# Performance work log

Hardware: AMD Instinct MI355X
Metric: run time of the kernel (lower is better)

Reference implementation:

```python
import jax, jax.numpy as jnp
import numpy as np

N, D = 32768, 256  # n_nodes, in_dim == mem_dim


def setup_inputs() -> dict:
    key = jax.random.key(0)
    ks = jax.random.split(key, 8)
    inputs = jax.random.normal(ks[0], (N, D), jnp.float32)
    state = jax.random.normal(ks[1], (1, D), jnp.float32)  # initial root cell state
    s = 1.0 / np.sqrt(D)  # pytorch default uniform init bound
    root_W = jax.random.uniform(ks[2], (D, D), jnp.float32, -s, s)
    root_b = jax.random.uniform(ks[3], (D,), jnp.float32, -s, s)
    W_ih = jax.random.uniform(ks[4], (4 * D, D), jnp.float32, -s, s)
    W_hh = jax.random.uniform(ks[5], (4 * D, D), jnp.float32, -s, s)
    b_ih = jax.random.uniform(ks[6], (4 * D,), jnp.float32, -s, s)
    b_hh = jax.random.uniform(ks[7], (4 * D,), jnp.float32, -s, s)
    # topologically ordered random tree: parents[i] < i, node 0 is root
    rng = np.random.default_rng(0)
    raw = rng.integers(0, N, size=N)
    parents = jnp.asarray(np.minimum(raw, np.maximum(np.arange(N) - 1, 0)).astype(np.int64))
    idx = jnp.arange(N, dtype=jnp.int64)  # node -> input row (tree.idx)
    return dict(inputs=inputs, state=state, root_W=root_W, root_b=root_b,
                W_ih=W_ih, W_hh=W_hh, b_ih=b_ih, b_hh=b_hh,
                parents=parents, idx=idx)


def reference(inputs, state, root_W, root_b, W_ih, W_hh, b_ih, b_hh, parents, idx):
    n, d = inputs.shape
    # root: tanh(Linear(inputs[root_idx])), cell state = given state
    h0 = jnp.tanh(inputs[idx[0]] @ root_W.T + root_b)
    c0 = state[0]
    H = jnp.zeros((n, d), inputs.dtype).at[0].set(h0)
    C = jnp.zeros((n, d), inputs.dtype).at[0].set(c0)

    def step(carry, i):
        H, C = carry
        p = parents[i]
        x = inputs[idx[i]]
        # torch nn.LSTMCell: gates = x W_ih^T + b_ih + h W_hh^T + b_hh
        gates = x @ W_ih.T + b_ih + H[p] @ W_hh.T + b_hh
        ig, fg, gg, og = jnp.split(gates, 4)
        c = jax.nn.sigmoid(fg) * C[p] + jax.nn.sigmoid(ig) * jnp.tanh(gg)
        h = jax.nn.sigmoid(og) * jnp.tanh(c)
        return (H.at[i].set(h), C.at[i].set(c)), None

    (H, C), _ = jax.lax.scan(step, (H, C), jnp.arange(1, n))
    # topdown_hidden_traversal: scatter each node's hidden into a [n_inputs, mem_dim] buffer
    hiddens = jnp.zeros((n, d), inputs.dtype).at[idx].set(H)
    # (root topdown_state, root topdown hidden, all hiddens)
    return C[0:1], H[0:1], hiddens
```

## Files before the change

kernel.cpp:

```cpp
#include <hip/hip_runtime.h>


#define NN 32768
#define DD 256
#define GP 1024
#define DSTR 16

typedef __attribute__((ext_vector_type(8))) short short8;
typedef __attribute__((ext_vector_type(4))) float float4_;

static __device__ __forceinline__ unsigned short f2bf(float f) {
    unsigned u = __builtin_bit_cast(unsigned, f);
    unsigned r = u + 0x7FFFu + ((u >> 16) & 1u);
    return (unsigned short)(r >> 16);
}
static __device__ __forceinline__ float bf2f(unsigned short u) {
    unsigned v = ((unsigned)u) << 16;
    return __builtin_bit_cast(float, v);
}
static __device__ __forceinline__ float sigf(float x) { return 1.0f / (1.0f + __expf(-x)); }
static __device__ __forceinline__ float tanh_(float x) { return 1.0f - 2.0f / (__expf(2.0f * x) + 1.0f); }

__global__ void k_init(int* cnt, int* cur, int* done, int* maxd) {
    int g = blockIdx.x * 256 + threadIdx.x;
    if (g < NN + 2) { cnt[g] = 0; cur[g] = 0; }
    if (g < (NN + 2) * DSTR) done[g] = 0;
    if (g == 0) maxd[0] = 0;
}

__global__ void k_root(const float* __restrict__ X, const float* __restrict__ state,
                       const float* __restrict__ rootW, const float* __restrict__ rootb,
                       const int* __restrict__ idx,
                       unsigned short* __restrict__ Hb, float* __restrict__ C, int* __restrict__ done) {
    const int t = threadIdx.x;
    const int row = idx[0];
    const float4_* xr = (const float4_*)(X + (size_t)row * DD);
    const float4_* wr = (const float4_*)(rootW + (size_t)t * DD);
    float acc = rootb[t];
    for (int k = 0; k < DD / 4; ++k) {
        float4_ a = xr[k], b = wr[k];
        acc += a[0] * b[0] + a[1] * b[1] + a[2] * b[2] + a[3] * b[3];
    }
    Hb[t] = f2bf(tanh_(acc));
    C[t] = state[t];
    __syncthreads();
    __threadfence();
    if (t == 0) __hip_atomic_store(&done[0], 8, __ATOMIC_RELEASE, __HIP_MEMORY_SCOPE_AGENT);
}

__global__ void k_dep_init(const int* __restrict__ parents, int* dep, int* jmp) {
    int i = blockIdx.x * 256 + threadIdx.x;
    if (i >= NN) return;
    dep[i] = (i == 0) ? 0 : 1;
    jmp[i] = (i == 0) ? 0 : parents[i];
}

__global__ void k_dep_step(const int* __restrict__ depA, const int* __restrict__ jmpA,
                           int* __restrict__ depB, int* __restrict__ jmpB) {
    int i = blockIdx.x * 256 + threadIdx.x;
    if (i >= NN) return;
    int j = jmpA[i];
    depB[i] = depA[i] + depA[j];
    jmpB[i] = jmpA[j];
}

__global__ void k_hist(const int* __restrict__ dep, int* cnt, int* maxd) {
    int i = blockIdx.x * 256 + threadIdx.x;
    if (i >= NN) return;
    int d = dep[i];
    atomicAdd(&cnt[d], 1);
    atomicMax(&maxd[0], d);
}

__global__ void k_scan(const int* __restrict__ cnt, int* __restrict__ off) {
    __shared__ int sums[256];
    const int tid = threadIdx.x;
    const int base = tid * 128;
    int s = 0;
    for (int k = 0; k < 128; ++k) s += cnt[base + k];
    sums[tid] = s;
    __syncthreads();
    if (tid == 0) {
        int run = 0;
        for (int t = 0; t < 256; ++t) { int tmp = sums[t]; sums[t] = run; run += tmp; }
    }
    __syncthreads();
    int run = sums[tid];
    for (int k = 0; k < 128; ++k) { off[base + k] = run; run += cnt[base + k]; }
    if (tid == 255) off[NN] = run;
}

__global__ void k_scatter(const int* __restrict__ dep, const int* __restrict__ off,
                          int* cur, int* __restrict__ lev) {
    int i = blockIdx.x * 256 + threadIdx.x;
    if (i >= NN) return;
    int d = dep[i];
    int pos = off[d] + atomicAdd(&cur[d], 1);
    lev[pos] = i;
}

__global__ __launch_bounds__(256, 1) void k_gx(
    const float* __restrict__ X, const float* __restrict__ Wih,
    const float* __restrict__ bih, const float* __restrict__ bhh,
    const int* __restrict__ idx, unsigned short* __restrict__ Gp) {
    __shared__ __align__(16) short bw_s[128 * 264];
    __shared__ float bias_s[128];
    const int tid = threadIdx.x;
    const int w = tid >> 6, l = tid & 63;
    const int lanelo = l & 15, quad = l >> 4;

    short8 a[2][8];
    #pragma unroll
    for (int ti = 0; ti < 2; ++ti) {
        int n = (blockIdx.x * 8 + w * 2 + ti) * 16 + lanelo;
        int row = idx[n];
        const float* xp = X + (size_t)row * DD + quad * 8;
        #pragma unroll
        for (int ks = 0; ks < 8; ++ks) {
            float4_ x0 = *(const float4_*)(xp + ks * 32);
            float4_ x1 = *(const float4_*)(xp + ks * 32 + 4);
            short8 s;
            s[0] = f2bf(x0[0]); s[1] = f2bf(x0[1]); s[2] = f2bf(x0[2]); s[3] = f2bf(x0[3]);
            s[4] = f2bf(x1[0]); s[5] = f2bf(x1[1]); s[6] = f2bf(x1[2]); s[7] = f2bf(x1[3]);
            a[ti][ks] = s;
        }
    }
    for (int gc = 0; gc < 8; ++gc) {
        __syncthreads();
        for (int e = tid; e < 128 * 64; e += 256) {
            int r = e >> 6, c4 = (e & 63) * 4;
            float4_ b = *(const float4_*)(Wih + (size_t)(gc * 128 + r) * DD + c4);
            unsigned short* pb = (unsigned short*)&bw_s[r * 264 + c4];
            pb[0] = f2bf(b[0]); pb[1] = f2bf(b[1]); pb[2] = f2bf(b[2]); pb[3] = f2bf(b[3]);
        }
        if (tid < 128) bias_s[tid] = bih[gc * 128 + tid] + bhh[gc * 128 + tid];
        __syncthreads();
        #pragma unroll
        for (int ntl = 0; ntl < 8; ++ntl) {
            float4_ acc0 = (float4_){0.f, 0.f, 0.f, 0.f};
            float4_ acc1 = (float4_){0.f, 0.f, 0.f, 0.f};
            #pragma unroll
            for (int ks = 0; ks < 8; ++ks) {
                short8 bf = *(const short8*)&bw_s[(ntl * 16 + lanelo) * 264 + ks * 32 + quad * 8];
                acc0 = __builtin_amdgcn_mfma_f32_16x16x32_bf16(a[0][ks], bf, acc0, 0, 0, 0);
                acc1 = __builtin_amdgcn_mfma_f32_16x16x32_bf16(a[1][ks], bf, acc1, 0, 0, 0);
            }
            float bia = bias_s[ntl * 16 + lanelo];
            int g = gc * 128 + ntl * 16 + lanelo;
            int nb0 = (blockIdx.x * 8 + w * 2) * 16 + quad * 4;
            #pragma unroll
            for (int r = 0; r < 4; ++r) {
                Gp[(size_t)(nb0 + r) * GP + g] = f2bf(acc0[r] + bia);
                Gp[(size_t)(nb0 + 16 + r) * GP + g] = f2bf(acc1[r] + bia);
            }
        }
    }
}

__global__ __launch_bounds__(256, 1) void k_tree2(
    const float* __restrict__ Whh,
    const int* __restrict__ parents,
    const int* __restrict__ off, const int* __restrict__ lev, const int* __restrict__ maxd_g,
    const unsigned short* __restrict__ Gp,
    unsigned short* __restrict__ Hb, float* __restrict__ C, int* __restrict__ done) {

    __shared__ __align__(16) short w_s[128 * 264];
    __shared__ __align__(16) short A_s[16 * 264];
    __shared__ __align__(16) float G_s[16 * 128];
    __shared__ __align__(16) float R_s[16 * 132];
    __shared__ int nd_s[16], par_s[16];

    const int tid = threadIdx.x;
    const int j = blockIdx.x & 7, grp = blockIdx.x >> 3;
    const int w = tid >> 6, l = tid & 63;
    const int lanelo = l & 15, quad = l >> 4;

    for (int e = tid; e < 128 * 64; e += 256) {
        int r = e >> 6, c4 = (e & 63) * 4;
        int G = ((r >> 5) * 256) + j * 32 + (r & 31);
        float4_ b = *(const float4_*)(Whh + (size_t)G * DD + c4);
        unsigned short* pb = (unsigned short*)&w_s[r * 264 + c4];
        pb[0] = f2bf(b[0]); pb[1] = f2bf(b[1]); pb[2] = f2bf(b[2]); pb[3] = f2bf(b[3]);
    }
    __syncthreads();

    const int maxd = maxd_g[0];
    int prev_lo = off[0], lo = off[1];
    for (int d = 1; d <= maxd; ++d) {
        const int hi = off[d + 1];
        const int tiles = (hi - lo + 15) >> 4;
        if (grp < tiles) {
            const int target = ((lo - prev_lo + 15) >> 4) << 3;
            int ndone = 0;
            for (int t = grp; t < tiles; t += 32) {
                const int base = lo + t * 16;
                if (tid < 16) {
                    int node = -1, p = 0;
                    if (base + tid < hi) { node = lev[base + tid]; p = parents[node]; }
                    nd_s[tid] = node; par_s[tid] = p;
                }
                __syncthreads();
                {
                    int m = tid >> 4, q8 = (tid & 15) * 8;
                    int seg = q8 >> 5, cc = q8 & 31;
                    float4_ g01 = (float4_){0.f, 0.f, 0.f, 0.f};
                    float4_ g23 = (float4_){0.f, 0.f, 0.f, 0.f};
                    if (nd_s[m] >= 0) {
                        const unsigned short* gp =
                            Gp + (size_t)nd_s[m] * GP + seg * 256 + j * 32 + cc;
                        short8 gv = *(const short8*)gp;
                        g01[0] = bf2f(gv[0]); g01[1] = bf2f(gv[1]); g01[2] = bf2f(gv[2]); g01[3] = bf2f(gv[3]);
                        g23[0] = bf2f(gv[4]); g23[1] = bf2f(gv[5]); g23[2] = bf2f(gv[6]); g23[3] = bf2f(gv[7]);
                    }
                    *(float4_*)&G_s[m * 128 + q8] = g01;
                    *(float4_*)&G_s[m * 128 + q8 + 4] = g23;
                }
                if (t == grp) {
                    if (tid == 0) {
                        while (__hip_atomic_load(&done[(d - 1) * DSTR], __ATOMIC_RELAXED,
                                                 __HIP_MEMORY_SCOPE_AGENT) < target)
                            __builtin_amdgcn_s_sleep(1);
                    }
                    __syncthreads();
                    __builtin_amdgcn_fence(__ATOMIC_ACQUIRE, "workgroup");
                }
                float cp0, cp1;
                {
                    int m0 = tid >> 5, c0 = tid & 31, col = j * 32 + c0;
                    cp0 = __hip_atomic_load(&C[(size_t)par_s[m0] * DD + col],
                                            __ATOMIC_RELAXED, __HIP_MEMORY_SCOPE_AGENT);
                    cp1 = __hip_atomic_load(&C[(size_t)par_s[m0 + 8] * DD + col],
                                            __ATOMIC_RELAXED, __HIP_MEMORY_SCOPE_AGENT);
                }
                {
                    const unsigned* HbU = (const unsigned*)Hb;
                    unsigned hv[8];
                    #pragma unroll
                    for (int k2 = 0; k2 < 8; ++k2) {
                        int e = tid + k2 * 256, m = e >> 7, cu = e & 127;
                        hv[k2] = (nd_s[m] >= 0)
                            ? __hip_atomic_load(&HbU[(size_t)par_s[m] * 128 + cu],
                                                __ATOMIC_RELAXED, __HIP_MEMORY_SCOPE_AGENT)
                            : 0u;
                    }
                    #pragma unroll
                    for (int k2 = 0; k2 < 8; ++k2) {
                        int e = tid + k2 * 256, m = e >> 7, cu = e & 127;
                        *(unsigned*)&A_s[m * 264 + cu * 2] = hv[k2];
                    }
                }
                __syncthreads();
                {
                    short8 af[8];
                    #pragma unroll
                    for (int ks = 0; ks < 8; ++ks)
                        af[ks] = *(const short8*)&A_s[lanelo * 264 + ks * 32 + quad * 8];
                    #pragma unroll
                    for (int ti = 0; ti < 2; ++ti) {
                        int ntl = w * 2 + ti;
                        float4_ acc = (float4_){0.f, 0.f, 0.f, 0.f};
                        #pragma unroll
                        for (int ks = 0; ks < 8; ++ks) {
                            short8 bf = *(const short8*)&w_s[(ntl * 16 + lanelo) * 264 + ks * 32 + quad * 8];
                            acc = __builtin_amdgcn_mfma_f32_16x16x32_bf16(af[ks], bf, acc, 0, 0, 0);
                        }
                        #pragma unroll
                        for (int r = 0; r < 4; ++r)
                            R_s[(quad * 4 + r) * 132 + ntl * 16 + lanelo] = acc[r];
                    }
                }
                __syncthreads();
                {
                    int m0 = tid >> 5, c = tid & 31, col = j * 32 + c;
                    #pragma unroll
                    for (int pass = 0; pass < 2; ++pass) {
                        int m = m0 + pass * 8;
                        float cp = pass ? cp1 : cp0;
                        float ig = R_s[m * 132 + c]      + G_s[m * 128 + c];
                        float fg = R_s[m * 132 + 32 + c] + G_s[m * 128 + 32 + c];
                        float gg = R_s[m * 132 + 64 + c] + G_s[m * 128 + 64 + c];
                        float og = R_s[m * 132 + 96 + c] + G_s[m * 128 + 96 + c];
                        float cn = sigf(fg) * cp + sigf(ig) * tanh_(gg);
                        float hn = sigf(og) * tanh_(cn);
                        int node = nd_s[m];
                        unsigned short hs = f2bf(hn);
                        unsigned pair = ((unsigned)hs) |
                                        (((unsigned)(unsigned short)__shfl_down((int)hs, 1)) << 16);
                        if (node >= 0) {
                            __hip_atomic_store(&C[(size_t)node * DD + col], cn,
                                               __ATOMIC_RELAXED, __HIP_MEMORY_SCOPE_AGENT);
                            if ((c & 1) == 0)
                                __hip_atomic_store(&((unsigned*)Hb)[(size_t)node * 128 + (col >> 1)],
                                                   pair, __ATOMIC_RELAXED, __HIP_MEMORY_SCOPE_AGENT);
                        }
                    }
                }
                ndone++;
                __syncthreads();
            }
            __builtin_amdgcn_fence(__ATOMIC_RELEASE, "workgroup");
            if (tid == 0)
                __hip_atomic_fetch_add(&done[d * DSTR], ndone,
                                       __ATOMIC_RELAXED, __HIP_MEMORY_SCOPE_AGENT);
        }
        prev_lo = lo; lo = hi;
    }
}

__global__ void k_out(const unsigned short* __restrict__ Hb, const float* __restrict__ C,
                      const int* __restrict__ idx, float* __restrict__ out) {
    const int b = blockIdx.x, t = threadIdx.x;
    if (b < NN) {
        int drow = idx[b];
        out[512 + (size_t)drow * DD + t] = bf2f(Hb[(size_t)b * DD + t]);
    } else {
        out[t] = C[t];
        out[DD + t] = bf2f(Hb[t]);
    }
}

extern "C" void kernel_launch(void* const* d_in, const int* in_sizes, int n_in,
                              void* d_out, int out_size, void* d_ws, size_t ws_size,
                              hipStream_t stream) {
    const float* X     = (const float*)d_in[0];
    const float* state = (const float*)d_in[1];
    const float* rootW = (const float*)d_in[2];
    const float* rootb = (const float*)d_in[3];
    const float* Wih   = (const float*)d_in[4];
    const float* Whh   = (const float*)d_in[5];
    const float* bih   = (const float*)d_in[6];
    const float* bhh   = (const float*)d_in[7];
    const int* parents = (const int*)d_in[8];
    const int* idx     = (const int*)d_in[9];

    float* C           = (float*)d_ws;
    unsigned short* Hb = (unsigned short*)(C + (size_t)NN * DD);
    unsigned short* Gp = Hb + (size_t)NN * DD;
    int* ip            = (int*)(Gp + (size_t)NN * GP);
    int* depA = ip;            ip += NN;
    int* jmpA = ip;            ip += NN;
    int* depB = ip;            ip += NN;
    int* jmpB = ip;            ip += NN;
    int* cnt  = ip;            ip += NN + 2;
    int* off  = ip;            ip += NN + 2;
    int* cur  = ip;            ip += NN + 2;
    int* lev  = ip;            ip += NN;
    int* done = ip;            ip += (NN + 2) * DSTR;
    int* maxd = ip;            ip += 4;
    float* out = (float*)d_out;

    k_init<<<dim3(((NN + 2) * DSTR + 255) / 256), dim3(256), 0, stream>>>(cnt, cur, done, maxd);
    k_root<<<dim3(1), dim3(256), 0, stream>>>(X, state, rootW, rootb, idx, Hb, C, done);

    k_dep_init<<<dim3(128), dim3(256), 0, stream>>>(parents, depA, jmpA);
    int* dA = depA; int* jA = jmpA; int* dB = depB; int* jB = jmpB;
    for (int it = 0; it < 15; ++it) {
        k_dep_step<<<dim3(128), dim3(256), 0, stream>>>(dA, jA, dB, jB);
        int* tp;
        tp = dA; dA = dB; dB = tp;
        tp = jA; jA = jB; jB = tp;
    }
    k_hist<<<dim3(128), dim3(256), 0, stream>>>(dA, cnt, maxd);
    k_scan<<<dim3(1), dim3(256), 0, stream>>>(cnt, off);
    k_scatter<<<dim3(128), dim3(256), 0, stream>>>(dA, off, cur, lev);

    k_gx<<<dim3(256), dim3(256), 0, stream>>>(X, Wih, bih, bhh, idx, Gp);
    k_tree2<<<dim3(256), dim3(256), 0, stream>>>(Whh, parents, off, lev, maxd, Gp, Hb, C, done);
    k_out<<<dim3(NN + 1), dim3(256), 0, stream>>>(Hb, C, idx, out);
}
```

Baseline: 1.765 ms.

## Replace per-level barrier with per-tile dataflow dependency waits in tree LSTM

The tree kernel no longer waits for a whole depth level to finish before starting the next. Each 16-node tile now waits only for the specific tiles holding its nodes' parents, tracked through per-tile done counters built by new scan/scatter/tile kernels. Parent hidden states are also loaded straight into MFMA A-fragments in registers instead of being staged through shared memory, which drops a barrier. The cost is extra preprocessing kernels and per-lane polling on several counters, and there is an unused bias load added to the tree kernel.

```diff
diff --git a/kernel.cpp b/kernel.cpp
--- a/kernel.cpp
+++ b/kernel.cpp
@@ -21,17 +21,16 @@
 static __device__ __forceinline__ float sigf(float x) { return 1.0f / (1.0f + __expf(-x)); }
 static __device__ __forceinline__ float tanh_(float x) { return 1.0f - 2.0f / (__expf(2.0f * x) + 1.0f); }
 
-__global__ void k_init(int* cnt, int* cur, int* done, int* maxd) {
+__global__ void k_init(int* cnt, int* cur, int* done2) {
     int g = blockIdx.x * 256 + threadIdx.x;
     if (g < NN + 2) { cnt[g] = 0; cur[g] = 0; }
-    if (g < (NN + 2) * DSTR) done[g] = 0;
-    if (g == 0) maxd[0] = 0;
+    if (g < (NN + 2) * DSTR) done2[g] = 0;
 }
 
 __global__ void k_root(const float* __restrict__ X, const float* __restrict__ state,
                        const float* __restrict__ rootW, const float* __restrict__ rootb,
                        const int* __restrict__ idx,
-                       unsigned short* __restrict__ Hb, float* __restrict__ C, int* __restrict__ done) {
+                       unsigned short* __restrict__ Hb, float* __restrict__ C, int* __restrict__ done2) {
     const int t = threadIdx.x;
     const int row = idx[0];
     const float4_* xr = (const float4_*)(X + (size_t)row * DD);
@@ -45,7 +44,7 @@
     C[t] = state[t];
     __syncthreads();
     __threadfence();
-    if (t == 0) __hip_atomic_store(&done[0], 8, __ATOMIC_RELEASE, __HIP_MEMORY_SCOPE_AGENT);
+    if (t == 0) __hip_atomic_store(&done2[0], 8, __ATOMIC_RELEASE, __HIP_MEMORY_SCOPE_AGENT);
 }
 
 __global__ void k_dep_init(const int* __restrict__ parents, int* dep, int* jmp) {
@@ -64,39 +63,57 @@
     jmpB[i] = jmpA[j];
 }
 
-__global__ void k_hist(const int* __restrict__ dep, int* cnt, int* maxd) {
+__global__ void k_hist(const int* __restrict__ dep, int* cnt) {
     int i = blockIdx.x * 256 + threadIdx.x;
     if (i >= NN) return;
-    int d = dep[i];
-    atomicAdd(&cnt[d], 1);
-    atomicMax(&maxd[0], d);
-}
-
-__global__ void k_scan(const int* __restrict__ cnt, int* __restrict__ off) {
-    __shared__ int sums[256];
+    atomicAdd(&cnt[dep[i]], 1);
+}
+
+__global__ void k_scan2(const int* __restrict__ cnt, int* __restrict__ off,
+                        int* __restrict__ tb, int* __restrict__ nt) {
+    __shared__ int sums[256], tsums[256];
     const int tid = threadIdx.x;
     const int base = tid * 128;
-    int s = 0;
-    for (int k = 0; k < 128; ++k) s += cnt[base + k];
-    sums[tid] = s;
+    int s = 0, st = 0;
+    for (int k = 0; k < 128; ++k) { int c = cnt[base + k]; s += c; st += (c + 15) >> 4; }
+    sums[tid] = s; tsums[tid] = st;
     __syncthreads();
     if (tid == 0) {
-        int run = 0;
-        for (int t = 0; t < 256; ++t) { int tmp = sums[t]; sums[t] = run; run += tmp; }
+        int run = 0, trun = 0;
+        for (int t = 0; t < 256; ++t) {
+            int a = sums[t]; sums[t] = run; run += a;
+            int b = tsums[t]; tsums[t] = trun; trun += b;
+        }
     }
     __syncthreads();
-    int run = sums[tid];
-    for (int k = 0; k < 128; ++k) { off[base + k] = run; run += cnt[base + k]; }
-    if (tid == 255) off[NN] = run;
-}
-
-__global__ void k_scatter(const int* __restrict__ dep, const int* __restrict__ off,
-                          int* cur, int* __restrict__ lev) {
+    int run = sums[tid], trun = tsums[tid];
+    for (int k = 0; k < 128; ++k) {
+        off[base + k] = run; tb[base + k] = trun;
+        run += cnt[base + k]; trun += (cnt[base + k] + 15) >> 4;
+    }
+    if (tid == 255) { off[NN] = run; tb[NN] = trun; nt[0] = trun; }
+}
+
+__global__ void k_scatter2(const int* __restrict__ dep, const int* __restrict__ off,
+                           const int* __restrict__ tb, int* cur,
+                           int* __restrict__ lev, int* __restrict__ tile_of) {
     int i = blockIdx.x * 256 + threadIdx.x;
     if (i >= NN) return;
     int d = dep[i];
     int pos = off[d] + atomicAdd(&cur[d], 1);
     lev[pos] = i;
+    tile_of[i] = tb[d] + ((pos - off[d]) >> 4);
+}
+
+__global__ void k_tiles(const int* __restrict__ off, const int* __restrict__ tb,
+                        int* __restrict__ tstart, int* __restrict__ tcount) {
+    int d = blockIdx.x * 256 + threadIdx.x;
+    if (d >= NN) return;
+    int lo = off[d], hi = off[d + 1], t0 = tb[d];
+    for (int k = 0; 16 * k < hi - lo; ++k) {
+        tstart[t0 + k] = lo + 16 * k;
+        tcount[t0 + k] = min(16, hi - lo - 16 * k);
+    }
 }
 
 __global__ __launch_bounds__(256, 1) void k_gx(
@@ -157,18 +174,20 @@
     }
 }
 
-__global__ __launch_bounds__(256, 1) void k_tree2(
+__global__ __launch_bounds__(256, 1) void k_tree4(
     const float* __restrict__ Whh,
     const int* __restrict__ parents,
-    const int* __restrict__ off, const int* __restrict__ lev, const int* __restrict__ maxd_g,
+    const int* __restrict__ tstart, const int* __restrict__ tcount,
+    const int* __restrict__ nt_g, const int* __restrict__ tile_of,
+    const int* __restrict__ lev,
     const unsigned short* __restrict__ Gp,
-    unsigned short* __restrict__ Hb, float* __restrict__ C, int* __restrict__ done) {
+    const float* __restrict__ bih, const float* __restrict__ bhh,
+    unsigned short* __restrict__ Hb, float* __restrict__ C, int* __restrict__ done2) {
 
     __shared__ __align__(16) short w_s[128 * 264];
-    __shared__ __align__(16) short A_s[16 * 264];
     __shared__ __align__(16) float G_s[16 * 128];
     __shared__ __align__(16) float R_s[16 * 132];
-    __shared__ int nd_s[16], par_s[16];
+    __shared__ float bias_s[128];
 
     const int tid = threadIdx.x;
     const int j = blockIdx.x & 7, grp = blockIdx.x >> 3;
@@ -182,128 +201,120 @@
         unsigned short* pb = (unsigned short*)&w_s[r * 264 + c4];
         pb[0] = f2bf(b[0]); pb[1] = f2bf(b[1]); pb[2] = f2bf(b[2]); pb[3] = f2bf(b[3]);
     }
+    if (tid < 128) {
+        int G = ((tid >> 5) * 256) + j * 32 + (tid & 31);
+        bias_s[tid] = bih[G] + bhh[G];
+    }
     __syncthreads();
 
-    const int maxd = maxd_g[0];
-    int prev_lo = off[0], lo = off[1];
-    for (int d = 1; d <= maxd; ++d) {
-        const int hi = off[d + 1];
-        const int tiles = (hi - lo + 15) >> 4;
-        if (grp < tiles) {
-            const int target = ((lo - prev_lo + 15) >> 4) << 3;
-            int ndone = 0;
-            for (int t = grp; t < tiles; t += 32) {
-                const int base = lo + t * 16;
-                if (tid < 16) {
-                    int node = -1, p = 0;
-                    if (base + tid < hi) { node = lev[base + tid]; p = parents[node]; }
-                    nd_s[tid] = node; par_s[tid] = p;
+    const int NT = nt_g[0];
+    for (int t = 1 + grp; t < NT; t += 32) {
+        const int base = tstart[t], count = tcount[t];
+        int node = -1, par = 0, ptile = 0;
+        if (lanelo < count) {
+            node = lev[base + lanelo];
+            par = parents[node];
+            ptile = tile_of[par];
+        }
+        {
+            int m = tid >> 4, q8 = (tid & 15) * 8;
+            int node_m = __shfl(node, (tid >> 4) & 15);
+            node_m = __shfl(node, m);
+            int seg = q8 >> 5, cc = q8 & 31;
+            float4_ g01 = (float4_){0.f, 0.f, 0.f, 0.f};
+            float4_ g23 = (float4_){0.f, 0.f, 0.f, 0.f};
+            if (node_m >= 0) {
+                const unsigned short* gp = Gp + (size_t)node_m * GP + seg * 256 + j * 32 + cc;
+                short8 gv = *(const short8*)gp;
+                g01[0] = bf2f(gv[0]); g01[1] = bf2f(gv[1]); g01[2] = bf2f(gv[2]); g01[3] = bf2f(gv[3]);
+                g23[0] = bf2f(gv[4]); g23[1] = bf2f(gv[5]); g23[2] = bf2f(gv[6]); g23[3] = bf2f(gv[7]);
+            }
+            *(float4_*)&G_s[m * 128 + q8] = g01;
+            *(float4_*)&G_s[m * 128 + q8 + 4] = g23;
+        }
+        if (w == 0) {
+            int ready = (node < 0);
+            while (true) {
+                if (!ready)
+                    ready = (__hip_atomic_load(&done2[(size_t)ptile * DSTR], __ATOMIC_RELAXED,
+                                               __HIP_MEMORY_SCOPE_AGENT) >= 8);
+                if (__all(ready)) break;
+                __builtin_amdgcn_s_sleep(1);
+            }
+        }
+        __syncthreads();
+        __builtin_amdgcn_sched_barrier(0);
+        __builtin_amdgcn_fence(__ATOMIC_ACQUIRE, "workgroup");
+        float cp0 = 0.f, cp1 = 0.f;
+        {
+            int m0 = tid >> 5, c = tid & 31, col = j * 32 + c;
+            int n0 = __shfl(node, m0 & 15), p0 = __shfl(par, m0 & 15);
+            int n1 = __shfl(node, (m0 + 8) & 15), p1 = __shfl(par, (m0 + 8) & 15);
+            if (n0 >= 0) cp0 = __hip_atomic_load(&C[(size_t)p0 * DD + col],
+                                                 __ATOMIC_RELAXED, __HIP_MEMORY_SCOPE_AGENT);
+            if (n1 >= 0) cp1 = __hip_atomic_load(&C[(size_t)p1 * DD + col],
+                                                 __ATOMIC_RELAXED, __HIP_MEMORY_SCOPE_AGENT);
+        }
+        short8 ah[8];
+        const unsigned long long* Hb64 = (const unsigned long long*)Hb;
+        #pragma unroll
+        for (int ks = 0; ks < 8; ++ks) {
+            unsigned long long q0 = 0ull, q1 = 0ull;
+            if (node >= 0) {
+                size_t b8 = (size_t)par * 64 + ks * 8 + quad * 2;
+                q0 = __hip_atomic_load(&Hb64[b8], __ATOMIC_RELAXED, __HIP_MEMORY_SCOPE_AGENT);
+                q1 = __hip_atomic_load(&Hb64[b8 + 1], __ATOMIC_RELAXED, __HIP_MEMORY_SCOPE_AGENT);
+            }
+            union { unsigned long long q[2]; short8 s; } u;
+            u.q[0] = q0; u.q[1] = q1;
+            ah[ks] = u.s;
+        }
+        {
+            #pragma unroll
+            for (int ti = 0; ti < 2; ++ti) {
+                int ntl = w * 2 + ti;
+                float4_ acc = (float4_){0.f, 0.f, 0.f, 0.f};
+                #pragma unroll
+                for (int ks = 0; ks < 8; ++ks) {
+                    short8 bf = *(const short8*)&w_s[(ntl * 16 + lanelo) * 264 + ks * 32 + quad * 8];
+                    acc = __builtin_amdgcn_mfma_f32_16x16x32_bf16(ah[ks], bf, acc, 0, 0, 0);
                 }
-                __syncthreads();
-                {
-                    int m = tid >> 4, q8 = (tid & 15) * 8;
-                    int seg = q8 >> 5, cc = q8 & 31;
-                    float4_ g01 = (float4_){0.f, 0.f, 0.f, 0.f};
-                    float4_ g23 = (float4_){0.f, 0.f, 0.f, 0.f};
-                    if (nd_s[m] >= 0) {
-                        const unsigned short* gp =
-                            Gp + (size_t)nd_s[m] * GP + seg * 256 + j * 32 + cc;
-                        short8 gv = *(const short8*)gp;
-                        g01[0] = bf2f(gv[0]); g01[1] = bf2f(gv[1]); g01[2] = bf2f(gv[2]); g01[3] = bf2f(gv[3]);
-                        g23[0] = bf2f(gv[4]); g23[1] = bf2f(gv[5]); g23[2] = bf2f(gv[6]); g23[3] = bf2f(gv[7]);
-                    }
-                    *(float4_*)&G_s[m * 128 + q8] = g01;
-                    *(float4_*)&G_s[m * 128 + q8 + 4] = g23;
+                #pragma unroll
+                for (int r = 0; r < 4; ++r)
+                    R_s[(quad * 4 + r) * 132 + ntl * 16 + lanelo] = acc[r];
+            }
+        }
+        __syncthreads();
+        {
+            int m0 = tid >> 5, c = tid & 31, col = j * 32 + c;
+            #pragma unroll
+            for (int pass = 0; pass < 2; ++pass) {
+                int m = m0 + pass * 8;
+                int nodem = __shfl(node, m & 15);
+                float cp = pass ? cp1 : cp0;
+                float ig = R_s[m * 132 + c]      + G_s[m * 128 + c];
+                float fg = R_s[m * 132 + 32 + c] + G_s[m * 128 + 32 + c];
+                float gg = R_s[m * 132 + 64 + c] + G_s[m * 128 + 64 + c];
+                float og = R_s[m * 132 + 96 + c] + G_s[m * 128 + 96 + c];
+                float cn = sigf(fg) * cp + sigf(ig) * tanh_(gg);
+                float hn = sigf(og) * tanh_(cn);
+                unsigned short hs = f2bf(hn);
+                unsigned pair = ((unsigned)hs) |
+                                (((unsigned)(unsigned short)__shfl_down((int)hs, 1)) << 16);
+                if (nodem >= 0) {
+                    __hip_atomic_store(&C[(size_t)nodem * DD + col], cn,
+                                       __ATOMIC_RELAXED, __HIP_MEMORY_SCOPE_AGENT);
+                    if ((c & 1) == 0)
+                        __hip_atomic_store(&((unsigned*)Hb)[(size_t)nodem * 128 + (col >> 1)],
+                                           pair, __ATOMIC_RELAXED, __HIP_MEMORY_SCOPE_AGENT);
                 }
-                if (t == grp) {
-                    if (tid == 0) {
-                        while (__hip_atomic_load(&done[(d - 1) * DSTR], __ATOMIC_RELAXED,
-                                                 __HIP_MEMORY_SCOPE_AGENT) < target)
-                            __builtin_amdgcn_s_sleep(1);
-                    }
-                    __syncthreads();
-                    __builtin_amdgcn_fence(__ATOMIC_ACQUIRE, "workgroup");
-                }
-                float cp0, cp1;
-                {
-                    int m0 = tid >> 5, c0 = tid & 31, col = j * 32 + c0;
-                    cp0 = __hip_atomic_load(&C[(size_t)par_s[m0] * DD + col],
-                                            __ATOMIC_RELAXED, __HIP_MEMORY_SCOPE_AGENT);
-                    cp1 = __hip_atomic_load(&C[(size_t)par_s[m0 + 8] * DD + col],
-                                            __ATOMIC_RELAXED, __HIP_MEMORY_SCOPE_AGENT);
-                }
-                {
-                    const unsigned* HbU = (const unsigned*)Hb;
-                    unsigned hv[8];
-                    #pragma unroll
-                    for (int k2 = 0; k2 < 8; ++k2) {
-                        int e = tid + k2 * 256, m = e >> 7, cu = e & 127;
-                        hv[k2] = (nd_s[m] >= 0)
-                            ? __hip_atomic_load(&HbU[(size_t)par_s[m] * 128 + cu],
-                                                __ATOMIC_RELAXED, __HIP_MEMORY_SCOPE_AGENT)
-                            : 0u;
-                    }
-                    #pragma unroll
-                    for (int k2 = 0; k2 < 8; ++k2) {
-                        int e = tid + k2 * 256, m = e >> 7, cu = e & 127;
-                        *(unsigned*)&A_s[m * 264 + cu * 2] = hv[k2];
-                    }
-                }
-                __syncthreads();
-                {
-                    short8 af[8];
-                    #pragma unroll
-                    for (int ks = 0; ks < 8; ++ks)
-                        af[ks] = *(const short8*)&A_s[lanelo * 264 + ks * 32 + quad * 8];
-                    #pragma unroll
-                    for (int ti = 0; ti < 2; ++ti) {
-                        int ntl = w * 2 + ti;
-                        float4_ acc = (float4_){0.f, 0.f, 0.f, 0.f};
-                        #pragma unroll
-                        for (int ks = 0; ks < 8; ++ks) {
-                            short8 bf = *(const short8*)&w_s[(ntl * 16 + lanelo) * 264 + ks * 32 + quad * 8];
-                            acc = __builtin_amdgcn_mfma_f32_16x16x32_bf16(af[ks], bf, acc, 0, 0, 0);
-                        }
-                        #pragma unroll
-                        for (int r = 0; r < 4; ++r)
-                            R_s[(quad * 4 + r) * 132 + ntl * 16 + lanelo] = acc[r];
-                    }
-                }
-                __syncthreads();
-                {
-                    int m0 = tid >> 5, c = tid & 31, col = j * 32 + c;
-                    #pragma unroll
-                    for (int pass = 0; pass < 2; ++pass) {
-                        int m = m0 + pass * 8;
-                        float cp = pass ? cp1 : cp0;
-                        float ig = R_s[m * 132 + c]      + G_s[m * 128 + c];
-                        float fg = R_s[m * 132 + 32 + c] + G_s[m * 128 + 32 + c];
-                        float gg = R_s[m * 132 + 64 + c] + G_s[m * 128 + 64 + c];
-                        float og = R_s[m * 132 + 96 + c] + G_s[m * 128 + 96 + c];
-                        float cn = sigf(fg) * cp + sigf(ig) * tanh_(gg);
-                        float hn = sigf(og) * tanh_(cn);
-                        int node = nd_s[m];
-                        unsigned short hs = f2bf(hn);
-                        unsigned pair = ((unsigned)hs) |
-                                        (((unsigned)(unsigned short)__shfl_down((int)hs, 1)) << 16);
-                        if (node >= 0) {
-                            __hip_atomic_store(&C[(size_t)node * DD + col], cn,
-                                               __ATOMIC_RELAXED, __HIP_MEMORY_SCOPE_AGENT);
-                            if ((c & 1) == 0)
-                                __hip_atomic_store(&((unsigned*)Hb)[(size_t)node * 128 + (col >> 1)],
-                                                   pair, __ATOMIC_RELAXED, __HIP_MEMORY_SCOPE_AGENT);
-                        }
-                    }
-                }
-                ndone++;
-                __syncthreads();
-            }
-            __builtin_amdgcn_fence(__ATOMIC_RELEASE, "workgroup");
-            if (tid == 0)
-                __hip_atomic_fetch_add(&done[d * DSTR], ndone,
-                                       __ATOMIC_RELAXED, __HIP_MEMORY_SCOPE_AGENT);
-        }
-        prev_lo = lo; lo = hi;
+            }
+        }
+        __builtin_amdgcn_fence(__ATOMIC_RELEASE, "workgroup");
+        __syncthreads();
+        if (tid == 0)
+            __hip_atomic_fetch_add(&done2[(size_t)t * DSTR], 1,
+                                   __ATOMIC_RELAXED, __HIP_MEMORY_SCOPE_AGENT);
     }
 }
 
@@ -337,20 +348,24 @@
     unsigned short* Hb = (unsigned short*)(C + (size_t)NN * DD);
     unsigned short* Gp = Hb + (size_t)NN * DD;
     int* ip            = (int*)(Gp + (size_t)NN * GP);
-    int* depA = ip;            ip += NN;
-    int* jmpA = ip;            ip += NN;
-    int* depB = ip;            ip += NN;
-    int* jmpB = ip;            ip += NN;
-    int* cnt  = ip;            ip += NN + 2;
-    int* off  = ip;            ip += NN + 2;
-    int* cur  = ip;            ip += NN + 2;
-    int* lev  = ip;            ip += NN;
-    int* done = ip;            ip += (NN + 2) * DSTR;
-    int* maxd = ip;            ip += 4;
+    int* depA    = ip; ip += NN;
+    int* jmpA    = ip; ip += NN;
+    int* depB    = ip; ip += NN;
+    int* jmpB    = ip; ip += NN;
+    int* cnt     = ip; ip += NN + 2;
+    int* off     = ip; ip += NN + 2;
+    int* tb      = ip; ip += NN + 2;
+    int* cur     = ip; ip += NN + 2;
+    int* lev     = ip; ip += NN;
+    int* tile_of = ip; ip += NN;
+    int* tstart  = ip; ip += NN;
+    int* tcount  = ip; ip += NN;
+    int* done2   = ip; ip += (NN + 2) * DSTR;
+    int* nt      = ip; ip += 4;
     float* out = (float*)d_out;
 
-    k_init<<<dim3(((NN + 2) * DSTR + 255) / 256), dim3(256), 0, stream>>>(cnt, cur, done, maxd);
-    k_root<<<dim3(1), dim3(256), 0, stream>>>(X, state, rootW, rootb, idx, Hb, C, done);
+    k_init<<<dim3(((NN + 2) * DSTR + 255) / 256), dim3(256), 0, stream>>>(cnt, cur, done2);
+    k_root<<<dim3(1), dim3(256), 0, stream>>>(X, state, rootW, rootb, idx, Hb, C, done2);
 
     k_dep_init<<<dim3(128), dim3(256), 0, stream>>>(parents, depA, jmpA);
     int* dA = depA; int* jA = jmpA; int* dB = depB; int* jB = jmpB;
@@ -360,11 +375,13 @@
         tp = dA; dA = dB; dB = tp;
         tp = jA; jA = jB; jB = tp;
     }
-    k_hist<<<dim3(128), dim3(256), 0, stream>>>(dA, cnt, maxd);
-    k_scan<<<dim3(1), dim3(256), 0, stream>>>(cnt, off);
-    k_scatter<<<dim3(128), dim3(256), 0, stream>>>(dA, off, cur, lev);
+    k_hist<<<dim3(128), dim3(256), 0, stream>>>(dA, cnt);
+    k_scan2<<<dim3(1), dim3(256), 0, stream>>>(cnt, off, tb, nt);
+    k_scatter2<<<dim3(128), dim3(256), 0, stream>>>(dA, off, tb, cur, lev, tile_of);
+    k_tiles<<<dim3(128), dim3(256), 0, stream>>>(off, tb, tstart, tcount);
 
     k_gx<<<dim3(256), dim3(256), 0, stream>>>(X, Wih, bih, bhh, idx, Gp);
-    k_tree2<<<dim3(256), dim3(256), 0, stream>>>(Whh, parents, off, lev, maxd, Gp, Hb, C, done);
+    k_tree4<<<dim3(256), dim3(256), 0, stream>>>(Whh, parents, tstart, tcount, nt, tile_of,
+                                                 lev, Gp, bih, bhh, Hb, C, done2);
     k_out<<<dim3(NN + 1), dim3(256), 0, stream>>>(Hb, C, idx, out);
 }
```

After: 2.253 ms. 1.28x slower.
